# Kernel optimization log

Measured on AMD Instinct MI355X. Metric: run time of the kernel, lower is better.

The kernel has to match this reference:

```python
import jax, jax.numpy as jnp
import numpy as np
import math

F = 32; NB = 8; MAXZ = 55; CUTOFF = 5.0; NIT = 3
B = 32; N = 32

def _cgc(j1, m1, j2, m2, J, M):
    if m1 + m2 != M or J < abs(j1 - j2) or J > j1 + j2: return 0.0
    f = math.factorial
    pref = (2*J+1)*f(J+j1-j2)*f(J-j1+j2)*f(j1+j2-J)/f(j1+j2+J+1)
    pref *= f(J+M)*f(J-M)*f(j1-m1)*f(j1+m1)*f(j2-m2)*f(j2+m2)
    s = 0.0
    for k in range(0, j1+j2+1):
        d = [j1+j2-J-k, j1-m1-k, j2+m2-k, J-j2+m1+k, J-j1-m2+k]
        if any(x < 0 for x in d): continue
        s += (-1)**k/(f(k)*f(d[0])*f(d[1])*f(d[2])*f(d[3])*f(d[4]))
    return math.sqrt(pref)*s

def _U(l):
    M = np.zeros((2*l+1, 2*l+1), dtype=np.complex128); M[l, l] = 1.0
    for m in range(1, l+1):
        M[l+m, l+m] = (-1)**m/math.sqrt(2); M[l+m, l-m] = 1/math.sqrt(2)
        M[l-m, l-m] = 1j/math.sqrt(2); M[l-m, l+m] = -1j*(-1)**m/math.sqrt(2)
    return M

def _build_cg():
    cg = np.zeros((9, 9, 9), dtype=np.float64)
    for l1 in range(3):
        for l2 in range(3):
            for l3 in range(3):
                if l3 < abs(l1-l2) or l3 > l1+l2: continue
                C = np.zeros((2*l1+1, 2*l2+1, 2*l3+1))
                for a, m1 in enumerate(range(-l1, l1+1)):
                    for b, m2 in enumerate(range(-l2, l2+1)):
                        for c, m3 in enumerate(range(-l3, l3+1)):
                            C[a, b, c] = _cgc(l1, m1, l2, m2, l3, m3)
                G = np.einsum('am,bn,co,mno->abc', _U(l1), _U(l2), np.conj(_U(l3)), C.astype(np.complex128))
                R = np.where(np.abs(G.imag) > np.abs(G.real), G.imag, G.real)
                cg[l1*l1:(l1+1)**2, l2*l2:(l2+1)**2, l3*l3:(l3+1)**2] = R
    return cg.astype(np.float32)

CG = jnp.asarray(_build_cg())
DM = np.array([0, 1, 1, 1, 2, 2, 2, 2, 2])
EVEN_B = jnp.asarray((DM % 2 == 0).astype(np.float32))
ODD_B = jnp.asarray((DM % 2 == 1).astype(np.float32))

def _degmask(maxdeg):
    return jnp.asarray((DM <= maxdeg).astype(np.float32))

def _sph(u):
    x, y, z = u[..., 0], u[..., 1], u[..., 2]
    s3 = math.sqrt(3.0)
    return jnp.stack([jnp.ones_like(x), y, z, x, s3*x*y, s3*y*z, 0.5*(3*z*z - 1.0), s3*x*z, 0.5*s3*(x*x - y*y)], axis=-1)

def _radial(r):
    f = 1.0/(1.0 + r)
    k = jnp.arange(NB, dtype=f.dtype)
    binom = jnp.asarray([math.comb(NB-1, i) for i in range(NB)], dtype=jnp.float32)
    rb = binom*(f[:, None]**k)*((1.0 - f[:, None])**(NB-1-k))
    u2 = (r/CUTOFF)**2
    cut = jnp.where(r < CUTOFF, jnp.exp(1.0 - 1.0/jnp.clip(1.0 - u2, 1e-6, None)), 0.0)
    return rb*cut[:, None]

def _dense(x, W, b):
    y = jnp.einsum('npmf,fg->npmg', x, W)
    return y.at[:, 0, 0, :].add(b)

def _silu(x):
    return x*jax.nn.sigmoid(x[:, :1, :1, :])

def _expand_path(Wp):  # (3,3,3,F) -> (9,9,9,F) by degree of each m index
    return Wp[DM[:, None, None], DM[None, :, None], DM[None, None, :]]

def _couple(x1, x2, Wp, maxdeg):
    cgw = CG[..., None]*_expand_path(Wp)
    def cp(a, b):
        return jnp.einsum('nabf,abcf->ncf', jnp.einsum('naf,nbf->nabf', a, b), cgw)
    p0 = cp(x1[:, 0], x2[:, 0]) + cp(x1[:, 1], x2[:, 1])
    p1 = cp(x1[:, 0], x2[:, 1]) + cp(x1[:, 1], x2[:, 0])
    return jnp.stack([p0, p1], axis=1)*_degmask(maxdeg)[None, None, :, None]

def _tensor_dense(x, W1, W2, Wp, maxdeg):
    u = jnp.einsum('npmf,fg->npmg', x, W1)
    v = jnp.einsum('npmf,fg->npmg', x, W2)
    return _couple(u, v, Wp, maxdeg)

def _message_pass(x, sh, rad, Wmp, dst, src, nseg, maxdeg):
    # g[e,b,f] = Y_b(r_hat_e) * (radial_e @ Wmp[deg(b)])
    g = sh[:, :, None]*jnp.einsum('en,bnf->ebf', rad, Wmp[DM])
    ge = g*EVEN_B[None, :, None]; go = g*ODD_B[None, :, None]
    xs = x[src]
    def cp(a, b):
        return jnp.einsum('eabf,abc->ecf', jnp.einsum('eaf,ebf->eabf', a, b), CG)
    y0 = cp(xs[:, 0], ge) + cp(xs[:, 1], go)
    y1 = cp(xs[:, 0], go) + cp(xs[:, 1], ge)
    msg = jnp.stack([y0, y1], axis=1)*_degmask(maxdeg)[None, None, :, None]
    return jax.ops.segment_sum(msg, dst, num_segments=nseg)

def _forward(atomic_numbers, positions, Ef, dst_idx, src_idx, batch_size,
             embed, Wmp, Wd, bd, Wt, Wtd1, Wtd2, Wtdp, Wh, bh, Wq,
             Wdip1, Wdip2, Wdipp, wdip, We, be, element_bias):
    Z = atomic_numbers.reshape(-1)
    pos = positions.reshape(-1, 3)
    Bv = int(batch_size); BNv = Z.shape[0]; Nn = BNv // Bv
    offsets = (jnp.arange(Bv, dtype=dst_idx.dtype)*Nn)
    dst = (dst_idx[None, :] + offsets[:, None]).reshape(-1)
    src = (src_idx[None, :] + offsets[:, None]).reshape(-1)
    batch_segments = jnp.repeat(jnp.arange(Bv, dtype=jnp.int32), Nn)
    disp = pos[src] - pos[dst]
    r = jnp.linalg.norm(disp, axis=-1)
    u = disp/(r[:, None] + 1e-10)
    sh = _sph(u); rad = _radial(r)
    # external field features: vector Ef in the degree-1 slots (m = 1..3)
    ef_rep = jnp.repeat(Ef, Nn, axis=0)
    xEF = jnp.zeros((BNv, 2, 9, F), dtype=pos.dtype).at[:, :, 1:4, :].set(ef_rep[:, None, :, None])
    # atomic-number embedding lives in the even scalar channel
    x = jnp.zeros((BNv, 2, 9, F), dtype=pos.dtype).at[:, 0, 0, :].set(embed[Z])
    for i in range(NIT):
        md = 2 if i < NIT - 1 else 0
        y = _message_pass(x, sh, rad, Wmp[i], dst, src, BNv, md)
        x = x + y
        x = _silu(x)
        x = _dense(x, Wd[i], bd[i])
        x = _silu(x)
        xEF = _couple(x, xEF, Wt[i], 2)
        x = x + xEF
        x = _tensor_dense(x, Wtd1[i], Wtd2[i], Wtdp[i], 2)
        x = x + y
    for i in range(4):
        x = _silu(_dense(x, Wh[i], bh[i]))
    x = _dense(x, Wh[4], bh[4])
    x_orig = x
    scal = x[:, 0, 0, :]
    charges = scal @ Wq
    # dipole head: proper tensors up to degree 1 -> TensorDense -> vector readout
    xd = jnp.zeros_like(x_orig)
    xd = xd.at[:, 0, 0, :].set(x_orig[:, 0, 0, :])
    xd = xd.at[:, 1, 1:4, :].set(x_orig[:, 1, 1:4, :])
    xd = _tensor_dense(xd, Wdip1, Wdip2, Wdipp, 1)
    atomic_dipoles = jnp.einsum('ncf,f->nc', xd[:, 1, 1:4, :], wdip)
    pos_b = pos.reshape(Bv, Nn, 3)
    q_b = charges.reshape(Bv, Nn)
    d_b = atomic_dipoles.reshape(Bv, Nn, 3)
    com = pos_b.mean(axis=1, keepdims=True)
    dipole = jnp.sum(q_b[:, :, None]*(pos_b - com), axis=1) + d_b.sum(axis=1)
    aE = scal @ We + be + element_bias[Z]
    energy = aE.reshape(Bv, Nn).sum(axis=1)
    pair = charges[src]*charges[dst]/(r + 1e-10)
    coul = jax.ops.segment_sum(pair, batch_segments[dst], num_segments=Bv)/2.0
    energy = energy + coul*14.399645
    return energy, dipole

def setup_inputs() -> dict:
    key = jax.random.key(0)
    ks = jax.random.split(key, 20)
    pos = jax.random.uniform(ks[0], (B, N, 3), dtype=jnp.float32)*8.0
    Z = jax.random.randint(ks[1], (B, N), 1, MAXZ + 1)
    Ef = jax.random.normal(ks[2], (B, 3), dtype=jnp.float32)*0.01
    ii, jj = np.meshgrid(np.arange(N), np.arange(N), indexing='ij')
    mask = ii != jj
    dst_idx = jnp.asarray(ii[mask].astype(np.int32))
    src_idx = jnp.asarray(jj[mask].astype(np.int32))
    s = 1.0/math.sqrt(F)
    def nrm(k, shape, sc=s):
        return jax.random.normal(k, shape, dtype=jnp.float32)*sc
    return {
        'atomic_numbers': Z, 'positions': pos, 'Ef': Ef,
        'dst_idx': dst_idx, 'src_idx': src_idx, 'batch_size': B,
        'embed': nrm(ks[3], (MAXZ + 1, F), 1.0),
        'Wmp': nrm(ks[4], (NIT, 3, NB, F)),
        'Wd': nrm(ks[5], (NIT, F, F)), 'bd': jnp.zeros((NIT, F), jnp.float32),
        'Wt': nrm(ks[6], (NIT, 3, 3, 3, F)),
        'Wtd1': nrm(ks[7], (NIT, F, F)), 'Wtd2': nrm(ks[8], (NIT, F, F)),
        'Wtdp': nrm(ks[9], (NIT, 3, 3, 3, F)),
        'Wh': nrm(ks[10], (5, F, F)), 'bh': jnp.zeros((5, F), jnp.float32),
        'Wq': nrm(ks[11], (F,), 0.1*s),
        'Wdip1': nrm(ks[12], (F, F)), 'Wdip2': nrm(ks[13], (F, F)),
        'Wdipp': nrm(ks[14], (3, 3, 3, F)), 'wdip': nrm(ks[15], (F,), 0.1*s),
        'We': nrm(ks[16], (F,), 0.1*s), 'be': jnp.zeros((), jnp.float32),
        'element_bias': nrm(ks[17], (MAXZ + 1,), 0.1),
    }

def reference(atomic_numbers, positions, Ef, dst_idx, src_idx, batch_size,
              embed, Wmp, Wd, bd, Wt, Wtd1, Wtd2, Wtdp, Wh, bh, Wq,
              Wdip1, Wdip2, Wdipp, wdip, We, be, element_bias):
    return _forward(atomic_numbers, positions, Ef, dst_idx, src_idx, batch_size,
                    embed, Wmp, Wd, bd, Wt, Wtd1, Wtd2, Wtdp, Wh, bh, Wq,
                    Wdip1, Wdip2, Wdipp, wdip, We, be, element_bias)
```

## Files before the change

### kernel.cpp

```cpp
#include <hip/hip_runtime.h>
#include <utility>
#include <type_traits>


namespace cgb {
constexpr double SQ2 = 1.4142135623730951;
constexpr double cabs_(double x){ return x < 0 ? -x : x; }
constexpr double fact(int n){ double r = 1.0; for (int i = 2; i <= n; ++i) r *= (double)i; return r; }
constexpr double csqrt(double x){
  if (x <= 0.0) return 0.0;
  double g = x > 1.0 ? x : 1.0;
  for (int i = 0; i < 48; ++i) g = 0.5 * (g + x / g);
  return g;
}
constexpr double cgc(int j1,int m1,int j2,int m2,int J,int M){
  if (m1 + m2 != M) return 0.0;
  int ad = j1 - j2; if (ad < 0) ad = -ad;
  if (J < ad || J > j1 + j2) return 0.0;
  double pref = (2.0*J+1.0) * fact(J+j1-j2) * fact(J-j1+j2) * fact(j1+j2-J) / fact(j1+j2+J+1);
  pref *= fact(J+M)*fact(J-M)*fact(j1-m1)*fact(j1+m1)*fact(j2-m2)*fact(j2+m2);
  double s = 0.0;
  for (int k = 0; k <= j1+j2; ++k){
    int d0=j1+j2-J-k, d1=j1-m1-k, d2=j2+m2-k, d3=J-j2+m1+k, d4=J-j1-m2+k;
    if (d0<0||d1<0||d2<0||d3<0||d4<0) continue;
    double t = 1.0/(fact(k)*fact(d0)*fact(d1)*fact(d2)*fact(d3)*fact(d4));
    s += (k & 1) ? -t : t;
  }
  return csqrt(pref) * s;
}
struct C2 { double re, im; };
struct URow { int n; int col[2]; C2 v[2]; };
constexpr URow urow(int l, int r){
  URow u{};
  if (r == l){ u.n = 1; u.col[0] = l; u.v[0] = C2{1.0, 0.0}; return u; }
  if (r > l){
    int m = r - l; double sg = (m & 1) ? -1.0 : 1.0;
    u.n = 2;
    u.col[0] = l + m; u.v[0] = C2{ sg / SQ2, 0.0 };
    u.col[1] = l - m; u.v[1] = C2{ 1.0 / SQ2, 0.0 };
    return u;
  }
  int m = l - r; double sg = (m & 1) ? -1.0 : 1.0;
  u.n = 2;
  u.col[0] = l - m; u.v[0] = C2{ 0.0, 1.0 / SQ2 };
  u.col[1] = l + m; u.v[1] = C2{ 0.0, -sg / SQ2 };
  return u;
}
struct Tab { float v[9][9][9]; };
constexpr Tab build(){
  Tab t{};
  for (int l1 = 0; l1 < 3; ++l1)
  for (int l2 = 0; l2 < 3; ++l2)
  for (int l3 = 0; l3 < 3; ++l3){
    int ad = l1 - l2; if (ad < 0) ad = -ad;
    if (l3 < ad || l3 > l1 + l2) continue;
    double C[5][5][5] = {};
    for (int m = 0; m < 2*l1+1; ++m)
      for (int n = 0; n < 2*l2+1; ++n){
        int o = (m - l1) + (n - l2) + l3;
        if (o < 0 || o > 2*l3) continue;
        C[m][n][o] = cgc(l1, m-l1, l2, n-l2, l3, o-l3);
      }
    for (int a = 0; a < 2*l1+1; ++a)
    for (int b = 0; b < 2*l2+1; ++b)
    for (int c = 0; c < 2*l3+1; ++c){
      URow ua = urow(l1,a), ub = urow(l2,b), uc = urow(l3,c);
      double gre = 0.0, gim = 0.0;
      for (int i = 0; i < ua.n; ++i)
      for (int j = 0; j < ub.n; ++j)
      for (int k = 0; k < uc.n; ++k){
        double Cv = C[ua.col[i]][ub.col[j]][uc.col[k]];
        if (Cv == 0.0) continue;
        double r1 = ua.v[i].re*ub.v[j].re - ua.v[i].im*ub.v[j].im;
        double i1 = ua.v[i].re*ub.v[j].im + ua.v[i].im*ub.v[j].re;
        double cr = uc.v[k].re, ci = -uc.v[k].im;
        gre += (r1*cr - i1*ci) * Cv;
        gim += (r1*ci + i1*cr) * Cv;
      }
      double r = (cabs_(gim) > cabs_(gre)) ? gim : gre;
      t.v[l1*l1+a][l2*l2+b][l3*l3+c] = (float)r;
    }
  }
  return t;
}
constexpr Tab CGT = build();
}

constexpr int DM_[9] = {0,1,1,1,2,2,2,2,2};

template<class F, int... Is>
__device__ __forceinline__ void sf_impl(F&& f, std::integer_sequence<int, Is...>){
  (f(std::integral_constant<int, Is>{}), ...);
}
template<int N, class F>
__device__ __forceinline__ void static_for(F&& f){
  sf_impl(static_cast<F&&>(f), std::make_integer_sequence<int, N>{});
}

__device__ __forceinline__ float rsum32(float v){
  #pragma unroll
  for (int s = 16; s > 0; s >>= 1) v += __shfl_xor(v, s, 32);
  return v;
}

__device__ __forceinline__ float dot32_lds(const float* sm, int xrow_off,
                                           const float (&wcol)[32]){
  float acc = 0.f;
  #pragma unroll
  for (int i = 0; i < 8; ++i){
    float4 xv = *reinterpret_cast<const float4*>(&sm[xrow_off + 4*i]);
    acc = fmaf(xv.x, wcol[4*i+0], acc);
    acc = fmaf(xv.y, wcol[4*i+1], acc);
    acc = fmaf(xv.z, wcol[4*i+2], acc);
    acc = fmaf(xv.w, wcol[4*i+3], acc);
  }
  return acc;
}

__device__ __forceinline__ void dense_hg(float* sm, int xoff,
                                         const float* __restrict__ W,
                                         int ooff, int f, int hg){
  float wcol[32];
  #pragma unroll
  for (int fp = 0; fp < 32; ++fp) wcol[fp] = W[fp*32 + f];
  for (int m = hg; m < 18; m += 8)
    sm[ooff + m*32 + f] = dot32_lds(sm, xoff + m*32, wcol);
}

__device__ __forceinline__ void dense_silu_hg(float* sm, int xoff,
                                              const float* __restrict__ W,
                                              const float* __restrict__ bias,
                                              int ooff, int f, int hg){
  float wcol[32];
  #pragma unroll
  for (int fp = 0; fp < 32; ++fp) wcol[fp] = W[fp*32 + f];
  float acc0 = dot32_lds(sm, xoff, wcol);
  float b = bias[f];
  float gate = 1.f / (1.f + expf(-(acc0 + b)));
  for (int m = hg; m < 18; m += 8){
    float acc = (m == 0) ? (acc0 + b) : dot32_lds(sm, xoff + m*32, wcol);
    sm[ooff + m*32 + f] = acc * gate;
  }
}

template<int OUTMODE>
__device__ __forceinline__ void couple_stage(float* sm, int x1o, int x2o,
                                             const float* __restrict__ Wp,
                                             int dsto, int addo,
                                             float* gout, float* gef,
                                             int f, int wv, int q){
  int r2a = x2o + q*9*32 + f;
  int r2b = x2o + (q^1)*9*32 + f;
  static_for<9>([&](auto C){
    constexpr int c = C.value;
    if ((c & 3) == wv){
      bool need = true;
      if constexpr (OUTMODE == 3) need = q ? (c >= 1 && c <= 3) : (c == 0);
      if (need){
        float out = 0.f;
        static_for<81>([&](auto AB){
          constexpr int a = AB.value / 9, b = AB.value % 9;
          constexpr float v = cgb::CGT.v[a][b][c];
          if constexpr (v != 0.0f){
            constexpr int path = (DM_[a]*3 + DM_[b])*3 + DM_[c];
            float w   = v * Wp[path*32 + f];
            float x10 = sm[x1o + a*32 + f];
            float x11 = sm[x1o + (9+a)*32 + f];
            out = fmaf(w, fmaf(x10, sm[r2a + b*32], x11*sm[r2b + b*32]), out);
          }
        });
        int row = (q*9 + c)*32 + f;
        if constexpr (OUTMODE == 0){
          sm[dsto + row] = out + sm[addo + row];
          if (gef) gef[row] = out;
        }
        if constexpr (OUTMODE == 1) gout[row] = out + sm[addo + row];
        if constexpr (OUTMODE == 3){
          int slot = q ? c : 0;
          sm[dsto + slot*32 + f] = out + sm[addo + row];
        }
      }
    }
  });
}

#define L_WL   0
#define L_XB   768
#define L_EB   1344
#define L_YB   1920
#define L_RED  2496
#define L_TOT  4800
#define L_HA   (L_RED)
#define L_HB   (L_RED + 128)
#define L_TU   (L_RED + 256)
#define L_TV   (L_RED + 384)

struct KParams {
  const float* POS; const int* Z; const float* Ef;
  const int* src;
  const float* embed;
  const float* Wmp; const float* Wd; const float* bd;
  const float* Wt; const float* Wtd1; const float* Wtd2; const float* Wtdp;
  const float* Wh; const float* bh; const float* Wq;
  const float* Wdip1; const float* Wdip2; const float* Wdipp; const float* wdip;
  const float* We; const float* be; const float* ebias;
  const float* Xc; float* Xn; float* XEF;
  float* Q; float* AE; float* AD;
};

template<int MODE>
__global__ __launch_bounds__(256) void k_iter(KParams p){
  __shared__ __align__(16) float sm[L_TOT];
  int tid = threadIdx.x;
  int f = tid & 31, hg = tid >> 5, wv = tid >> 6, q = (tid >> 5) & 1;
  int n = ((blockIdx.x & 7) << 7) | (blockIdx.x >> 3);
  int bi = n >> 5, d = n & 31;

  for (int j = tid; j < 768; j += 256) sm[L_WL+j] = p.Wmp[j];
  if constexpr (MODE == 0){
    float e3[3] = { p.Ef[bi*3+0], p.Ef[bi*3+1], p.Ef[bi*3+2] };
    for (int j2 = tid; j2 < 576; j2 += 256){
      int m = (j2 >> 5) % 9;
      sm[L_EB + j2] = (m >= 1 && m <= 3) ? e3[m-1] : 0.f;
    }
  } else {
    const float* erow = p.XEF + (size_t)n*576;
    for (int j2 = tid; j2 < 576; j2 += 256) sm[L_EB+j2] = erow[j2];
  }
  __syncthreads();

  float pdx = p.POS[n*3+0], pdy = p.POS[n*3+1], pdz = p.POS[n*3+2];
  float acc[2][9];
  #pragma unroll
  for (int pp = 0; pp < 2; ++pp)
    #pragma unroll
    for (int c = 0; c < 9; ++c) acc[pp][c] = 0.0f;

  #pragma unroll
  for (int k = 0; k < 4; ++k){
    int t = hg + 8*k;
    if (t < 31){
      int ei = d*31 + t;
      int s = bi*32 + p.src[ei];
      float dx = p.POS[s*3+0] - pdx;
      float dy = p.POS[s*3+1] - pdy;
      float dz = p.POS[s*3+2] - pdz;
      float r  = sqrtf(dx*dx + dy*dy + dz*dz);
      float inv = 1.0f / (r + 1e-10f);
      float x = dx*inv, y = dy*inv, z = dz*inv;
      const float s3 = 1.7320508075688772f;
      float sh[9];
      sh[0] = 1.0f; sh[1] = y; sh[2] = z; sh[3] = x;
      sh[4] = s3*x*y; sh[5] = s3*y*z; sh[6] = 0.5f*(3.0f*z*z - 1.0f);
      sh[7] = s3*x*z; sh[8] = 0.5f*s3*(x*x - y*y);
      float fr = 1.0f / (1.0f + r);
      float om = 1.0f - fr;
      float frk[8]; frk[0] = 1.0f;
      #pragma unroll
      for (int kk = 1; kk < 8; ++kk) frk[kk] = frk[kk-1]*fr;
      float omk[8]; omk[0] = 1.0f;
      #pragma unroll
      for (int kk = 1; kk < 8; ++kk) omk[kk] = omk[kk-1]*om;
      const float bin[8] = {1.f,7.f,21.f,35.f,35.f,21.f,7.f,1.f};
      float u2 = (r*0.2f)*(r*0.2f);
      float cut = 0.0f;
      if (r < 5.0f){
        float den = fmaxf(1.0f - u2, 1e-6f);
        cut = expf(1.0f - 1.0f/den);
      }
      float rad[8];
      #pragma unroll
      for (int kk = 0; kk < 8; ++kk) rad[kk] = bin[kk]*frk[kk]*omk[7-kk]*cut;

      float wt0 = 0.f, wt1 = 0.f, wt2 = 0.f;
      #pragma unroll
      for (int nb = 0; nb < 8; ++nb){
        wt0 = fmaf(rad[nb], sm[L_WL + (0*8+nb)*32 + f], wt0);
        wt1 = fmaf(rad[nb], sm[L_WL + (1*8+nb)*32 + f], wt1);
        wt2 = fmaf(rad[nb], sm[L_WL + (2*8+nb)*32 + f], wt2);
      }
      float g[9];
      g[0] = sh[0]*wt0;
      g[1] = sh[1]*wt1; g[2] = sh[2]*wt1; g[3] = sh[3]*wt1;
      g[4] = sh[4]*wt2; g[5] = sh[5]*wt2; g[6] = sh[6]*wt2;
      g[7] = sh[7]*wt2; g[8] = sh[8]*wt2;

      if constexpr (MODE == 0){
        float x00 = p.embed[p.Z[s]*32 + f];
        static_for<9>([&](auto C){
          constexpr int c = C.value;
          constexpr int pb = DM_[c] & 1;
          acc[pb][c] = fmaf(g[c], x00, acc[pb][c]);
        });
      } else {
        const float* xp = p.Xc + (size_t)s*576 + f;
        static_for<9>([&](auto A){
          constexpr int a = A.value;
          float x0a = xp[a*32];
          float x1a = xp[(9+a)*32];
          static_for<81>([&](auto BC){
            constexpr int b = BC.value / 9, c = BC.value % 9;
            constexpr float v = cgb::CGT.v[a][b][c];
            if constexpr (v != 0.0f){
              constexpr int pb = DM_[b] & 1;
              float tg = v * g[b];
              acc[0][c] = fmaf(tg, pb ? x1a : x0a, acc[0][c]);
              acc[1][c] = fmaf(tg, pb ? x0a : x1a, acc[1][c]);
            }
          });
        });
      }
    }
  }
  #pragma unroll
  for (int pp = 0; pp < 2; ++pp)
    #pragma unroll
    for (int c = 0; c < 9; ++c) acc[pp][c] += __shfl_xor(acc[pp][c], 32);
  if ((tid & 63) < 32){
    #pragma unroll
    for (int pp = 0; pp < 2; ++pp)
      #pragma unroll
      for (int c = 0; c < 9; ++c) sm[L_RED + wv*576 + (pp*9+c)*32 + f] = acc[pp][c];
  }
  __syncthreads();

  {
    const float* xrow = (MODE == 0) ? nullptr : (p.Xc + (size_t)n*576);
    int zn = 0;
    if constexpr (MODE == 0) zn = p.Z[n];
    for (int j2 = tid; j2 < 576; j2 += 256){
      int jm = (j2 >> 5) % 9;
      int ff = j2 & 31;
      float y = sm[L_RED+j2] + sm[L_RED+576+j2] + sm[L_RED+1152+j2] + sm[L_RED+1728+j2];
      if (MODE == 2 && jm != 0) y = 0.f;
      float y0 = sm[L_RED+ff] + sm[L_RED+576+ff] + sm[L_RED+1152+ff] + sm[L_RED+1728+ff];
      float xv, x0;
      if constexpr (MODE == 0){
        xv = (j2 < 32) ? p.embed[zn*32 + j2] : 0.f;
        x0 = p.embed[zn*32 + ff];
      } else {
        xv = xrow[j2];
        x0 = xrow[ff];
      }
      float gate = 1.f / (1.f + expf(-(x0 + y0)));
      sm[L_YB + j2] = y;
      sm[L_XB + j2] = (xv + y) * gate;
    }
  }
  __syncthreads();

  dense_silu_hg(sm, L_XB, p.Wd, p.bd, L_RED, f, hg);
  __syncthreads();

  {
    float* erow = (MODE < 2) ? (p.XEF + (size_t)n*576) : nullptr;
    couple_stage<0>(sm, L_RED, L_EB, p.Wt, L_XB, L_RED, nullptr, erow, f, wv, q);
  }
  __syncthreads();

  dense_hg(sm, L_XB, p.Wtd1, L_RED + 576,  f, hg);
  dense_hg(sm, L_XB, p.Wtd2, L_RED + 1152, f, hg);
  __syncthreads();

  if constexpr (MODE < 2){
    couple_stage<1>(sm, L_RED + 576, L_RED + 1152, p.Wtdp, 0, L_YB,
                    p.Xn + (size_t)n*576, nullptr, f, wv, q);
    return;
  } else {
    couple_stage<3>(sm, L_RED + 576, L_RED + 1152, p.Wtdp, L_HA, L_YB,
                    nullptr, nullptr, f, wv, q);
  }
  __syncthreads();

  #pragma unroll
  for (int k = 0; k < 5; ++k){
    int srco = (k & 1) ? L_HB : L_HA;
    int dsto = (k & 1) ? L_HA : L_HB;
    if (hg < 4){
      float wcol[32];
      #pragma unroll
      for (int fp = 0; fp < 32; ++fp) wcol[fp] = p.Wh[k*1024 + fp*32 + f];
      float acc0 = dot32_lds(sm, srco, wcol);
      float b = p.bh[k*32 + f];
      float accr = (hg == 0) ? acc0 : dot32_lds(sm, srco + hg*32, wcol);
      float val = accr + ((hg == 0) ? b : 0.f);
      if (k < 4) val *= 1.f / (1.f + expf(-(acc0 + b)));
      sm[dsto + hg*32 + f] = val;
    }
    __syncthreads();
  }

  {
    int mat = hg >> 2;
    int slot = hg & 3;
    const float* W = mat ? p.Wdip2 : p.Wdip1;
    float wcol[32];
    #pragma unroll
    for (int fp = 0; fp < 32; ++fp) wcol[fp] = W[fp*32 + f];
    float acc2 = dot32_lds(sm, L_HB + slot*32, wcol);
    sm[(mat ? L_TV : L_TU) + slot*32 + f] = acc2;
  }
  __syncthreads();

  if (tid < 32){
    float scal = sm[L_HB + f];
    float qv = rsum32(scal * p.Wq[f]);
    float ae = rsum32(scal * p.We[f]) + p.be[0] + p.ebias[p.Z[n]];
    float u00 = sm[L_TU + f], v00 = sm[L_TV + f];
    float wp4  = p.Wdipp[4*32 + f];
    float wp10 = p.Wdipp[10*32 + f];
    float wd = p.wdip[f];
    float ad[3];
    #pragma unroll
    for (int c = 1; c <= 3; ++c){
      float p1 = wp4*u00*sm[L_TV + c*32 + f] + wp10*sm[L_TU + c*32 + f]*v00;
      ad[c-1] = rsum32(p1 * wd);
    }
    if (f == 0){
      p.Q[n] = qv;
      p.AE[n] = ae;
      p.AD[3*n+0] = ad[0]; p.AD[3*n+1] = ad[1]; p.AD[3*n+2] = ad[2];
    }
  }
}

__global__ __launch_bounds__(64) void k_final(const float* __restrict__ Q,
                                              const float* __restrict__ AE,
                                              const float* __restrict__ AD,
                                              const float* __restrict__ POS,
                                              const int* __restrict__ dst_idx,
                                              const int* __restrict__ src_idx,
                                              float* __restrict__ out,
                                              int Nn, int Eb, int Bv){
  __shared__ float qs[32];
  __shared__ float ps[32][3];
  int b = blockIdx.x, tid = threadIdx.x;
  float q = 0.f, ae = 0.f, px = 0.f, py = 0.f, pz = 0.f, ax = 0.f, ay = 0.f, az = 0.f;
  if (tid < Nn){
    int n = b*Nn + tid;
    q  = Q[n]; ae = AE[n];
    px = POS[n*3+0]; py = POS[n*3+1]; pz = POS[n*3+2];
    ax = AD[3*n+0]; ay = AD[3*n+1]; az = AD[3*n+2];
    qs[tid] = q;
    ps[tid][0] = px; ps[tid][1] = py; ps[tid][2] = pz;
  }
  __syncthreads();
  float invN = 1.0f / (float)Nn;
  float cx = rsum32(px) * invN;
  float cy = rsum32(py) * invN;
  float cz = rsum32(pz) * invN;
  float dipx = rsum32(q*(px - cx) + ax);
  float dipy = rsum32(q*(py - cy) + ay);
  float dipz = rsum32(q*(pz - cz) + az);
  float sae  = rsum32(ae);

  float cl = 0.0f;
  for (int e = tid; e < Eb; e += 64){
    int dd = dst_idx[e], ss = src_idx[e];
    float dx = ps[ss][0] - ps[dd][0];
    float dy = ps[ss][1] - ps[dd][1];
    float dz = ps[ss][2] - ps[dd][2];
    float r = sqrtf(dx*dx + dy*dy + dz*dz);
    cl += qs[ss]*qs[dd] / (r + 1e-10f);
  }
  #pragma unroll
  for (int s = 32; s > 0; s >>= 1) cl += __shfl_xor(cl, s, 64);

  if (tid == 0){
    out[b] = sae + 0.5f*cl*14.399645f;
    out[Bv + b*3 + 0] = dipx;
    out[Bv + b*3 + 1] = dipy;
    out[Bv + b*3 + 2] = dipz;
  }
}

extern "C" void kernel_launch(void* const* d_in, const int* in_sizes, int n_in,
                              void* d_out, int out_size, void* d_ws, size_t ws_size,
                              hipStream_t stream) {
  (void)n_in; (void)out_size; (void)ws_size;
  const int*   Z     = (const int*)  d_in[0];
  const float* POS   = (const float*)d_in[1];
  const float* Ef    = (const float*)d_in[2];
  const int*   dst   = (const int*)  d_in[3];
  const int*   src   = (const int*)  d_in[4];
  const float* embed = (const float*)d_in[6];
  const float* Wmp   = (const float*)d_in[7];
  const float* Wd    = (const float*)d_in[8];
  const float* bd    = (const float*)d_in[9];
  const float* Wt    = (const float*)d_in[10];
  const float* Wtd1  = (const float*)d_in[11];
  const float* Wtd2  = (const float*)d_in[12];
  const float* Wtdp  = (const float*)d_in[13];
  const float* Wh    = (const float*)d_in[14];
  const float* bh    = (const float*)d_in[15];
  const float* Wq    = (const float*)d_in[16];
  const float* Wdip1 = (const float*)d_in[17];
  const float* Wdip2 = (const float*)d_in[18];
  const float* Wdipp = (const float*)d_in[19];
  const float* wdip  = (const float*)d_in[20];
  const float* We    = (const float*)d_in[21];
  const float* be    = (const float*)d_in[22];
  const float* ebias = (const float*)d_in[23];

  const int BN = in_sizes[0];
  const int Bv = in_sizes[2] / 3;
  const int Nn = BN / Bv;
  const int Eb = in_sizes[3];

  float* wsf = (float*)d_ws;
  float* Xa  = wsf;
  float* Xb  = Xa  + (size_t)BN*576;
  float* XEF = Xb  + (size_t)BN*576;
  float* Qb  = XEF + (size_t)BN*576;
  float* AEb = Qb  + BN;
  float* AD  = AEb + BN;

  KParams p{};
  p.POS = POS; p.Z = Z; p.Ef = Ef; p.src = src; p.embed = embed;
  p.Wh = Wh; p.bh = bh; p.Wq = Wq;
  p.Wdip1 = Wdip1; p.Wdip2 = Wdip2; p.Wdipp = Wdipp; p.wdip = wdip;
  p.We = We; p.be = be; p.ebias = ebias;
  p.Q = Qb; p.AE = AEb; p.AD = AD;

  p.Wmp = Wmp; p.Wd = Wd; p.bd = bd; p.Wt = Wt;
  p.Wtd1 = Wtd1; p.Wtd2 = Wtd2; p.Wtdp = Wtdp;
  p.Xc = Xa; p.Xn = Xa; p.XEF = XEF;
  k_iter<0><<<BN, 256, 0, stream>>>(p);

  p.Wmp = Wmp + 768; p.Wd = Wd + 1024; p.bd = bd + 32; p.Wt = Wt + 864;
  p.Wtd1 = Wtd1 + 1024; p.Wtd2 = Wtd2 + 1024; p.Wtdp = Wtdp + 864;
  p.Xc = Xa; p.Xn = Xb;
  k_iter<1><<<BN, 256, 0, stream>>>(p);

  p.Wmp = Wmp + 2*768; p.Wd = Wd + 2*1024; p.bd = bd + 2*32; p.Wt = Wt + 2*864;
  p.Wtd1 = Wtd1 + 2*1024; p.Wtd2 = Wtd2 + 2*1024; p.Wtdp = Wtdp + 2*864;
  p.Xc = Xb; p.Xn = Xa;
  k_iter<2><<<BN, 256, 0, stream>>>(p);

  k_final<<<Bv, 64, 0, stream>>>(Qb, AEb, AD, POS, dst, src,
                                 (float*)d_out, Nn, Eb, Bv);
}
```

Measured before the change: 89.59 us.

## Double k_iter block to 512 threads and precompute edge geometry in LDS

Doubles the per-node block from 256 to 512 threads and redistributes work. Edges now go 2 per half-warp group instead of 4, the couple stage splits output channels across 8 groups, and the two dense layers run concurrently on separate halves of the block. Edge geometry (spherical harmonics, radial basis, source index) is computed once per edge by the first warp and stored in LDS, overlapping with the weight loads done by the other warps. This shortens the per-thread serial chain, but raises LDS use and makes the reduction sum eight partial buffers, which may lower occupancy.

```diff
diff --git a/kernel.cpp b/kernel.cpp
--- a/kernel.cpp
+++ b/kernel.cpp
@@ -117,27 +117,27 @@
   return acc;
 }
 
-__device__ __forceinline__ void dense_hg(float* sm, int xoff,
+__device__ __forceinline__ void dense_h8(float* sm, int xoff,
                                          const float* __restrict__ W,
-                                         int ooff, int f, int hg){
+                                         int ooff, int f, int h8){
   float wcol[32];
   #pragma unroll
   for (int fp = 0; fp < 32; ++fp) wcol[fp] = W[fp*32 + f];
-  for (int m = hg; m < 18; m += 8)
+  for (int m = h8; m < 18; m += 8)
     sm[ooff + m*32 + f] = dot32_lds(sm, xoff + m*32, wcol);
 }
 
-__device__ __forceinline__ void dense_silu_hg(float* sm, int xoff,
-                                              const float* __restrict__ W,
-                                              const float* __restrict__ bias,
-                                              int ooff, int f, int hg){
+__device__ __forceinline__ void dense_silu_h16(float* sm, int xoff,
+                                               const float* __restrict__ W,
+                                               const float* __restrict__ bias,
+                                               int ooff, int f, int hg){
   float wcol[32];
   #pragma unroll
   for (int fp = 0; fp < 32; ++fp) wcol[fp] = W[fp*32 + f];
   float acc0 = dot32_lds(sm, xoff, wcol);
   float b = bias[f];
   float gate = 1.f / (1.f + expf(-(acc0 + b)));
-  for (int m = hg; m < 18; m += 8){
+  for (int m = hg; m < 18; m += 16){
     float acc = (m == 0) ? (acc0 + b) : dot32_lds(sm, xoff + m*32, wcol);
     sm[ooff + m*32 + f] = acc * gate;
   }
@@ -148,12 +148,12 @@
                                              const float* __restrict__ Wp,
                                              int dsto, int addo,
                                              float* gout, float* gef,
-                                             int f, int wv, int q){
+                                             int f, int cg, int q){
   int r2a = x2o + q*9*32 + f;
   int r2b = x2o + (q^1)*9*32 + f;
   static_for<9>([&](auto C){
     constexpr int c = C.value;
-    if ((c & 3) == wv){
+    if ((c & 7) == cg){
       bool need = true;
       if constexpr (OUTMODE == 3) need = q ? (c >= 1 && c <= 3) : (c == 0);
       if (need){
@@ -185,11 +185,12 @@
 }
 
 #define L_WL   0
-#define L_XB   768
-#define L_EB   1344
-#define L_YB   1920
-#define L_RED  2496
-#define L_TOT  4800
+#define L_GEO  768
+#define L_XB   1328
+#define L_EB   1904
+#define L_YB   2480
+#define L_RED  3056
+#define L_TOT  7664
 #define L_HA   (L_RED)
 #define L_HB   (L_RED + 128)
 #define L_TU   (L_RED + 256)
@@ -209,27 +210,65 @@
 };
 
 template<int MODE>
-__global__ __launch_bounds__(256) void k_iter(KParams p){
+__global__ __launch_bounds__(512) void k_iter(KParams p){
   __shared__ __align__(16) float sm[L_TOT];
   int tid = threadIdx.x;
-  int f = tid & 31, hg = tid >> 5, wv = tid >> 6, q = (tid >> 5) & 1;
+  int f = tid & 31, hg = tid >> 5;
+  int cg = hg >> 1, q = hg & 1;
+  int wv = tid >> 6;
   int n = ((blockIdx.x & 7) << 7) | (blockIdx.x >> 3);
   int bi = n >> 5, d = n & 31;
 
-  for (int j = tid; j < 768; j += 256) sm[L_WL+j] = p.Wmp[j];
-  if constexpr (MODE == 0){
-    float e3[3] = { p.Ef[bi*3+0], p.Ef[bi*3+1], p.Ef[bi*3+2] };
-    for (int j2 = tid; j2 < 576; j2 += 256){
-      int m = (j2 >> 5) % 9;
-      sm[L_EB + j2] = (m >= 1 && m <= 3) ? e3[m-1] : 0.f;
-    }
+  if (tid < 31){
+    int t = tid;
+    int s = bi*32 + p.src[d*31 + t];
+    float dx = p.POS[s*3+0] - p.POS[n*3+0];
+    float dy = p.POS[s*3+1] - p.POS[n*3+1];
+    float dz = p.POS[s*3+2] - p.POS[n*3+2];
+    float r  = sqrtf(dx*dx + dy*dy + dz*dz);
+    float inv = 1.0f / (r + 1e-10f);
+    float x = dx*inv, y = dy*inv, z = dz*inv;
+    const float s3 = 1.7320508075688772f;
+    float* gp = &sm[L_GEO + t*18];
+    gp[0] = 1.0f; gp[1] = y; gp[2] = z; gp[3] = x;
+    gp[4] = s3*x*y; gp[5] = s3*y*z; gp[6] = 0.5f*(3.0f*z*z - 1.0f);
+    gp[7] = s3*x*z; gp[8] = 0.5f*s3*(x*x - y*y);
+    float fr = 1.0f / (1.0f + r);
+    float om = 1.0f - fr;
+    float frk[8]; frk[0] = 1.0f;
+    #pragma unroll
+    for (int kk = 1; kk < 8; ++kk) frk[kk] = frk[kk-1]*fr;
+    float omk[8]; omk[0] = 1.0f;
+    #pragma unroll
+    for (int kk = 1; kk < 8; ++kk) omk[kk] = omk[kk-1]*om;
+    const float bin[8] = {1.f,7.f,21.f,35.f,35.f,21.f,7.f,1.f};
+    float u2 = (r*0.2f)*(r*0.2f);
+    float cut = 0.0f;
+    if (r < 5.0f){
+      float den = fmaxf(1.0f - u2, 1e-6f);
+      cut = expf(1.0f - 1.0f/den);
+    }
+    #pragma unroll
+    for (int kk = 0; kk < 8; ++kk) gp[9+kk] = bin[kk]*frk[kk]*omk[7-kk]*cut;
+    gp[17] = __int_as_float(s);
   } else {
-    const float* erow = p.XEF + (size_t)n*576;
-    for (int j2 = tid; j2 < 576; j2 += 256) sm[L_EB+j2] = erow[j2];
-  }
-  __syncthreads();
-
-  float pdx = p.POS[n*3+0], pdy = p.POS[n*3+1], pdz = p.POS[n*3+2];
+    int t2 = tid - 32;
+    if (t2 >= 0){
+      for (int j = t2; j < 768; j += 480) sm[L_WL+j] = p.Wmp[j];
+      if constexpr (MODE == 0){
+        float e3[3] = { p.Ef[bi*3+0], p.Ef[bi*3+1], p.Ef[bi*3+2] };
+        for (int j2 = t2; j2 < 576; j2 += 480){
+          int m = (j2 >> 5) % 9;
+          sm[L_EB + j2] = (m >= 1 && m <= 3) ? e3[m-1] : 0.f;
+        }
+      } else {
+        const float* erow = p.XEF + (size_t)n*576;
+        for (int j2 = t2; j2 < 576; j2 += 480) sm[L_EB+j2] = erow[j2];
+      }
+    }
+  }
+  __syncthreads();
+
   float acc[2][9];
   #pragma unroll
   for (int pp = 0; pp < 2; ++pp)
@@ -237,53 +276,24 @@
     for (int c = 0; c < 9; ++c) acc[pp][c] = 0.0f;
 
   #pragma unroll
-  for (int k = 0; k < 4; ++k){
-    int t = hg + 8*k;
+  for (int k = 0; k < 2; ++k){
+    int t = hg + 16*k;
     if (t < 31){
-      int ei = d*31 + t;
-      int s = bi*32 + p.src[ei];
-      float dx = p.POS[s*3+0] - pdx;
-      float dy = p.POS[s*3+1] - pdy;
-      float dz = p.POS[s*3+2] - pdz;
-      float r  = sqrtf(dx*dx + dy*dy + dz*dz);
-      float inv = 1.0f / (r + 1e-10f);
-      float x = dx*inv, y = dy*inv, z = dz*inv;
-      const float s3 = 1.7320508075688772f;
-      float sh[9];
-      sh[0] = 1.0f; sh[1] = y; sh[2] = z; sh[3] = x;
-      sh[4] = s3*x*y; sh[5] = s3*y*z; sh[6] = 0.5f*(3.0f*z*z - 1.0f);
-      sh[7] = s3*x*z; sh[8] = 0.5f*s3*(x*x - y*y);
-      float fr = 1.0f / (1.0f + r);
-      float om = 1.0f - fr;
-      float frk[8]; frk[0] = 1.0f;
-      #pragma unroll
-      for (int kk = 1; kk < 8; ++kk) frk[kk] = frk[kk-1]*fr;
-      float omk[8]; omk[0] = 1.0f;
-      #pragma unroll
-      for (int kk = 1; kk < 8; ++kk) omk[kk] = omk[kk-1]*om;
-      const float bin[8] = {1.f,7.f,21.f,35.f,35.f,21.f,7.f,1.f};
-      float u2 = (r*0.2f)*(r*0.2f);
-      float cut = 0.0f;
-      if (r < 5.0f){
-        float den = fmaxf(1.0f - u2, 1e-6f);
-        cut = expf(1.0f - 1.0f/den);
-      }
-      float rad[8];
-      #pragma unroll
-      for (int kk = 0; kk < 8; ++kk) rad[kk] = bin[kk]*frk[kk]*omk[7-kk]*cut;
-
+      const float* gp = &sm[L_GEO + t*18];
       float wt0 = 0.f, wt1 = 0.f, wt2 = 0.f;
       #pragma unroll
       for (int nb = 0; nb < 8; ++nb){
-        wt0 = fmaf(rad[nb], sm[L_WL + (0*8+nb)*32 + f], wt0);
-        wt1 = fmaf(rad[nb], sm[L_WL + (1*8+nb)*32 + f], wt1);
-        wt2 = fmaf(rad[nb], sm[L_WL + (2*8+nb)*32 + f], wt2);
+        float rv = gp[9+nb];
+        wt0 = fmaf(rv, sm[L_WL + (0*8+nb)*32 + f], wt0);
+        wt1 = fmaf(rv, sm[L_WL + (1*8+nb)*32 + f], wt1);
+        wt2 = fmaf(rv, sm[L_WL + (2*8+nb)*32 + f], wt2);
       }
       float g[9];
-      g[0] = sh[0]*wt0;
-      g[1] = sh[1]*wt1; g[2] = sh[2]*wt1; g[3] = sh[3]*wt1;
-      g[4] = sh[4]*wt2; g[5] = sh[5]*wt2; g[6] = sh[6]*wt2;
-      g[7] = sh[7]*wt2; g[8] = sh[8]*wt2;
+      g[0] = gp[0]*wt0;
+      g[1] = gp[1]*wt1; g[2] = gp[2]*wt1; g[3] = gp[3]*wt1;
+      g[4] = gp[4]*wt2; g[5] = gp[5]*wt2; g[6] = gp[6]*wt2;
+      g[7] = gp[7]*wt2; g[8] = gp[8]*wt2;
+      int s = __float_as_int(gp[17]);
 
       if constexpr (MODE == 0){
         float x00 = p.embed[p.Z[s]*32 + f];
@@ -328,12 +338,16 @@
     const float* xrow = (MODE == 0) ? nullptr : (p.Xc + (size_t)n*576);
     int zn = 0;
     if constexpr (MODE == 0) zn = p.Z[n];
-    for (int j2 = tid; j2 < 576; j2 += 256){
+    for (int j2 = tid; j2 < 576; j2 += 512){
       int jm = (j2 >> 5) % 9;
       int ff = j2 & 31;
-      float y = sm[L_RED+j2] + sm[L_RED+576+j2] + sm[L_RED+1152+j2] + sm[L_RED+1728+j2];
+      float y = 0.f, y0 = 0.f;
+      #pragma unroll
+      for (int w = 0; w < 8; ++w){
+        y  += sm[L_RED + w*576 + j2];
+        y0 += sm[L_RED + w*576 + ff];
+      }
       if (MODE == 2 && jm != 0) y = 0.f;
-      float y0 = sm[L_RED+ff] + sm[L_RED+576+ff] + sm[L_RED+1152+ff] + sm[L_RED+1728+ff];
       float xv, x0;
       if constexpr (MODE == 0){
         xv = (j2 < 32) ? p.embed[zn*32 + j2] : 0.f;
@@ -349,26 +363,26 @@
   }
   __syncthreads();
 
-  dense_silu_hg(sm, L_XB, p.Wd, p.bd, L_RED, f, hg);
+  dense_silu_h16(sm, L_XB, p.Wd, p.bd, L_RED, f, hg);
   __syncthreads();
 
   {
     float* erow = (MODE < 2) ? (p.XEF + (size_t)n*576) : nullptr;
-    couple_stage<0>(sm, L_RED, L_EB, p.Wt, L_XB, L_RED, nullptr, erow, f, wv, q);
-  }
-  __syncthreads();
-
-  dense_hg(sm, L_XB, p.Wtd1, L_RED + 576,  f, hg);
-  dense_hg(sm, L_XB, p.Wtd2, L_RED + 1152, f, hg);
+    couple_stage<0>(sm, L_RED, L_EB, p.Wt, L_XB, L_RED, nullptr, erow, f, cg, q);
+  }
+  __syncthreads();
+
+  if (hg < 8) dense_h8(sm, L_XB, p.Wtd1, L_RED + 576,  f, hg);
+  else        dense_h8(sm, L_XB, p.Wtd2, L_RED + 1152, f, hg - 8);
   __syncthreads();
 
   if constexpr (MODE < 2){
     couple_stage<1>(sm, L_RED + 576, L_RED + 1152, p.Wtdp, 0, L_YB,
-                    p.Xn + (size_t)n*576, nullptr, f, wv, q);
+                    p.Xn + (size_t)n*576, nullptr, f, cg, q);
     return;
   } else {
     couple_stage<3>(sm, L_RED + 576, L_RED + 1152, p.Wtdp, L_HA, L_YB,
-                    nullptr, nullptr, f, wv, q);
+                    nullptr, nullptr, f, cg, q);
   }
   __syncthreads();
 
@@ -390,7 +404,7 @@
     __syncthreads();
   }
 
-  {
+  if (hg < 8){
     int mat = hg >> 2;
     int slot = hg & 3;
     const float* W = mat ? p.Wdip2 : p.Wdip1;
@@ -525,17 +539,17 @@
   p.Wmp = Wmp; p.Wd = Wd; p.bd = bd; p.Wt = Wt;
   p.Wtd1 = Wtd1; p.Wtd2 = Wtd2; p.Wtdp = Wtdp;
   p.Xc = Xa; p.Xn = Xa; p.XEF = XEF;
-  k_iter<0><<<BN, 256, 0, stream>>>(p);
+  k_iter<0><<<BN, 512, 0, stream>>>(p);
 
   p.Wmp = Wmp + 768; p.Wd = Wd + 1024; p.bd = bd + 32; p.Wt = Wt + 864;
   p.Wtd1 = Wtd1 + 1024; p.Wtd2 = Wtd2 + 1024; p.Wtdp = Wtdp + 864;
   p.Xc = Xa; p.Xn = Xb;
-  k_iter<1><<<BN, 256, 0, stream>>>(p);
+  k_iter<1><<<BN, 512, 0, stream>>>(p);
 
   p.Wmp = Wmp + 2*768; p.Wd = Wd + 2*1024; p.bd = bd + 2*32; p.Wt = Wt + 2*864;
   p.Wtd1 = Wtd1 + 2*1024; p.Wtd2 = Wtd2 + 2*1024; p.Wtdp = Wtdp + 2*864;
   p.Xc = Xb; p.Xn = Xa;
-  k_iter<2><<<BN, 256, 0, stream>>>(p);
+  k_iter<2><<<BN, 512, 0, stream>>>(p);
 
   k_final<<<Bv, 64, 0, stream>>>(Qb, AEb, AD, POS, dst, src,
                                  (float*)d_out, Nn, Eb, Bv);
```

After: 99.95 us. 1.12x slower.
